# Performance work log

Hardware: AMD Instinct MI355X
Metric: run time of the kernel (lower is better)

The kernel has to match this reference:

```python
import jax, jax.numpy as jnp
import numpy as np

N, E, D, H = 100000, 1600000, 128, 128


def setup_inputs() -> dict:
    key = jax.random.key(0)
    ks = jax.random.split(key, 7)
    x = jax.random.normal(ks[0], (N, D), dtype=jnp.float32)
    edge_index = jax.random.randint(ks[1], (2, E), 0, N, dtype=jnp.int64)
    edge_weight = jax.random.uniform(ks[2], (E,), dtype=jnp.float32)
    s = 1.0 / np.sqrt(D)
    W0 = jax.random.normal(ks[3], (D, H), dtype=jnp.float32) * s
    b0 = jnp.zeros((H,), dtype=jnp.float32)
    W1 = jax.random.normal(ks[4], (H, H), dtype=jnp.float32) * (1.0 / np.sqrt(H))
    b1 = jnp.zeros((H,), dtype=jnp.float32)
    return {"x": x, "edge_weight": edge_weight, "W0": W0, "b0": b0,
            "W1": W1, "b1": b1, "edge_index": edge_index}


def reference(x, edge_weight, W0, b0, W1, b1, edge_index):
    src, dst = edge_index[0], edge_index[1]
    n = x.shape[0]
    # gcn_norm with self-loops (fill_value=1): deg includes the self-loop weight
    deg = jax.ops.segment_sum(edge_weight, dst, num_segments=n) + 1.0  # [N]
    dis = jnp.where(deg > 0, jax.lax.rsqrt(deg), 0.0)                  # deg^-1/2
    norm = dis[src] * edge_weight * dis[dst]                           # [E]
    self_coef = dis * dis                                              # self-loop norm = 1/deg

    def gcn_layer(h, W, b):
        hW = h @ W                                                     # [N,H]
        agg = jax.ops.segment_sum(norm[:, None] * hW[src], dst, num_segments=n)
        agg = agg + self_coef[:, None] * hW                            # self-loop term
        return jax.nn.relu(agg + b)

    h1 = gcn_layer(x, W0, b0)
    h2 = gcn_layer(h1, W1, b1)
    return jnp.concatenate([h1, h2], axis=1)  # [N, 2H]
```

## Files before the change

### kernel.cpp

```cpp
#include <hip/hip_runtime.h>
#include <hip/hip_fp16.h>


typedef unsigned int u32;
typedef _Float16 f16;
typedef f16 f16x8 __attribute__((ext_vector_type(8)));
typedef float f32x4 __attribute__((ext_vector_type(4)));

__global__ __launch_bounds__(256) void k_wfrag(const float* __restrict__ W0,
                                               const float* __restrict__ W1,
                                               __half* __restrict__ Wf) {
    int idx = blockIdx.x * 256 + threadIdx.x;
    const float* W = (idx < 2048) ? W0 : W1;
    int id = idx & 2047;
    int l = id & 63, nt = (id >> 6) & 7, ks = id >> 9;
    int nn = nt * 16 + (l & 15);
    int kb = ks * 32 + ((l >> 4) & 3) * 4;
    union { int4 v; __half h[8]; } pk;
#pragma unroll
    for (int j = 0; j < 8; ++j) {
        int k = kb + (j & 3) + 16 * (j >> 2);
        pk.h[j] = __float2half(W[k * 128 + nn]);
    }
    *(int4*)(Wf + (size_t)idx * 8) = pk.v;
}

__device__ __forceinline__ void gemm_body(const float* __restrict__ A, int lda,
                                          const __half* __restrict__ Wf,
                                          __half* __restrict__ C, int n,
                                          int bid, int t) {
    const int w2 = t >> 6, l = t & 63;
    const int node = bid * 64 + w2 * 16 + (l & 15);
    const int koff = ((l >> 4) & 3) * 4;
    const bool ok = node < n;
    const float* ap = A + (size_t)(ok ? node : 0) * lda;

    f16x8 af[4];
#pragma unroll
    for (int ks = 0; ks < 4; ++ks) {
        float4 a0 = make_float4(0.f, 0.f, 0.f, 0.f), a1 = a0;
        if (ok) {
            a0 = *(const float4*)(ap + ks * 32 + koff);
            a1 = *(const float4*)(ap + ks * 32 + koff + 16);
        }
        f16x8 h;
        h[0] = (f16)a0.x; h[1] = (f16)a0.y; h[2] = (f16)a0.z; h[3] = (f16)a0.w;
        h[4] = (f16)a1.x; h[5] = (f16)a1.y; h[6] = (f16)a1.z; h[7] = (f16)a1.w;
        af[ks] = h;
    }

    f32x4 acc[8];
#pragma unroll
    for (int i = 0; i < 8; ++i) acc[i] = (f32x4){0.f, 0.f, 0.f, 0.f};

#pragma unroll
    for (int ks = 0; ks < 4; ++ks) {
#pragma unroll
        for (int nt = 0; nt < 8; ++nt) {
            f16x8 wf = *(const f16x8*)(Wf + ((size_t)(ks * 8 + nt) * 64 + l) * 8);
            acc[nt] = __builtin_amdgcn_mfma_f32_16x16x32_f16(wf, af[ks], acc[nt], 0, 0, 0);
        }
    }

    if (ok) {
        const int c0 = ((l >> 4) & 3) * 4;
#pragma unroll
        for (int nt = 0; nt < 8; ++nt) {
            union { short4 s4; __half h[4]; } pk;
#pragma unroll
            for (int r2 = 0; r2 < 4; ++r2) pk.h[r2] = __float2half(acc[nt][r2]);
            *(short4*)(C + (size_t)node * 128 + nt * 16 + c0) = pk.s4;
        }
    }
}

__global__ __launch_bounds__(256) void k_p1gemm(const int* __restrict__ dst,
                                                u32* __restrict__ H,
                                                int e, int NB, int nch,
                                                const float* __restrict__ A, int lda,
                                                const __half* __restrict__ Wf,
                                                __half* __restrict__ C, int n) {
    const int bid = blockIdx.x, t = threadIdx.x;
    if (bid >= nch) {
        gemm_body(A, lda, Wf, C, n, bid - nch, t);
        return;
    }
    __shared__ u32 lcnt[512];
    lcnt[t] = 0; lcnt[t + 256] = 0;
    __syncthreads();
    int i0 = bid * 4096 + t;
#pragma unroll
    for (int u = 0; u < 16; ++u) {
        int i = i0 + u * 256;
        if (i < e) atomicAdd(&lcnt[(u32)dst[i] >> 9], 1u);
    }
    __syncthreads();
    for (int b = t; b < NB; b += 256) H[(size_t)b * nch + bid] = lcnt[b];
}

__global__ __launch_bounds__(256) void k_scan1(u32* data, u32* sums, int n) {
    __shared__ u32 tmp[256];
    int gid = blockIdx.x * 256 + threadIdx.x;
    u32 v = (gid < n) ? data[gid] : 0;
    tmp[threadIdx.x] = v;
    __syncthreads();
    for (int off = 1; off < 256; off <<= 1) {
        u32 t = (threadIdx.x >= off) ? tmp[threadIdx.x - off] : 0;
        __syncthreads();
        tmp[threadIdx.x] += t;
        __syncthreads();
    }
    if (gid < n) data[gid] = tmp[threadIdx.x] - v;
    if (threadIdx.x == 255) sums[blockIdx.x] = tmp[255];
}

__global__ __launch_bounds__(512) void k_scan2(u32* sums, int nb) {
    __shared__ u32 tmp[512];
    u32 v = (threadIdx.x < nb) ? sums[threadIdx.x] : 0;
    tmp[threadIdx.x] = v;
    __syncthreads();
    for (int off = 1; off < 512; off <<= 1) {
        u32 t = (threadIdx.x >= off) ? tmp[threadIdx.x - off] : 0;
        __syncthreads();
        tmp[threadIdx.x] += t;
        __syncthreads();
    }
    if (threadIdx.x < nb) sums[threadIdx.x] = tmp[threadIdx.x] - v;
}

__global__ __launch_bounds__(256) void k_scan3(u32* data, const u32* sums, int n) {
    int gid = blockIdx.x * 256 + threadIdx.x;
    if (gid < n) data[gid] += sums[blockIdx.x];
}

__global__ __launch_bounds__(256) void k_p2(const int* __restrict__ src,
                                            const int* __restrict__ dst,
                                            const float* __restrict__ w,
                                            const u32* __restrict__ H,
                                            int2* __restrict__ tmp,
                                            int e, int NB, int nch) {
    __shared__ u32 lcnt[512];
    __shared__ u32 lbase[512];
    const int t = threadIdx.x, bid = blockIdx.x;
    lcnt[t] = 0; lcnt[t + 256] = 0;
    __syncthreads();
    for (int b = t; b < NB; b += 256) lbase[b] = H[(size_t)b * nch + bid];
    __syncthreads();
    int i0 = bid * 4096 + t;
#pragma unroll
    for (int u = 0; u < 16; ++u) {
        int i = i0 + u * 256;
        if (i < e) {
            int d = dst[i];
            u32 b = (u32)d >> 9;
            u32 lr = atomicAdd(&lcnt[b], 1u);
            tmp[lbase[b] + lr] = make_int2(src[i] | ((d & 511) << 17),
                                           __float_as_int(w[i]));
        }
    }
}

__global__ __launch_bounds__(512) void k_p3a(const int2* __restrict__ tmp,
                                             const u32* __restrict__ H,
                                             int* __restrict__ rowstart,
                                             float* __restrict__ dis,
                                             int e, int n, int NB, int nch) {
    const int bid = blockIdx.x, t = threadIdx.x;
    __shared__ u32 cnt[512];
    __shared__ u32 degx[512];
    __shared__ u32 stmp[512];

    cnt[t] = 0; degx[t] = 0;
    __syncthreads();

    const int bs = (int)H[(size_t)bid * nch];
    const int be = (bid + 1 < NB) ? (int)H[(size_t)(bid + 1) * nch] : e;

    for (int j = bs + t; j < be; j += 512) {
        int2 r = tmp[j];
        u32 low = ((u32)r.x >> 17) & 511u;
        atomicAdd(&cnt[low], 1u);
        atomicAdd(&degx[low], (u32)(__int_as_float(r.y) * 1048576.0f + 0.5f));
    }
    __syncthreads();

    u32 v = cnt[t];
    stmp[t] = v;
    __syncthreads();
    for (int o = 1; o < 512; o <<= 1) {
        u32 x = (t >= o) ? stmp[t - o] : 0u;
        __syncthreads();
        stmp[t] += x;
        __syncthreads();
    }

    const int node = bid * 512 + t;
    if (node < n) {
        rowstart[node] = bs + (int)(stmp[t] - v);
        dis[node] = rsqrtf(1.0f + (float)degx[t] * (1.0f / 1048576.0f));
    }
}

__global__ __launch_bounds__(512) void k_p3b(const int2* __restrict__ tmp,
                                             const u32* __restrict__ H,
                                             const int* __restrict__ rowstart,
                                             const float* __restrict__ dis,
                                             int2* __restrict__ ep,
                                             int e, int n, int NB, int nch) {
    const int bid = blockIdx.x, t = threadIdx.x;
    __shared__ u32 cur[512];
    const int node = bid * 512 + t;
    cur[t] = (node < n) ? (u32)rowstart[node] : 0u;
    __syncthreads();

    const int bs = (int)H[(size_t)bid * nch];
    const int be = (bid + 1 < NB) ? (int)H[(size_t)(bid + 1) * nch] : e;

    for (int j = bs + t; j < be; j += 512) {
        int2 r = tmp[j];
        u32 low = ((u32)r.x >> 17) & 511u;
        int s = r.x & 0x1FFFF;
        float wd = __int_as_float(r.y) * dis[s];
        u32 p = atomicAdd(&cur[low], 1u);
        ep[p] = make_int2(s, __float_as_int(wd));
    }
}

__global__ __launch_bounds__(256) void k_gemm(const float* __restrict__ A, int lda,
                                              const __half* __restrict__ Wf,
                                              __half* __restrict__ C, int n) {
    gemm_body(A, lda, Wf, C, n, blockIdx.x, threadIdx.x);
}

__global__ __launch_bounds__(256) void k_agg(const __half* __restrict__ hW,
                                             const int2* __restrict__ ep,
                                             const int* __restrict__ rowstart,
                                             const float* __restrict__ dis,
                                             const float* __restrict__ bias,
                                             float* __restrict__ outcol,
                                             int n, int e) {
    int wid = blockIdx.x * 4 + (threadIdx.x >> 6);
    int lane = threadIdx.x & 63;
    if (wid >= n) return;

    int start = rowstart[wid];
    int end   = (wid == n - 1) ? e : rowstart[wid + 1];
    start = __builtin_amdgcn_readfirstlane(start);
    end   = __builtin_amdgcn_readfirstlane(end);

    const float dd = dis[wid];
    float2 h = __half22float2(*(const __half2*)(hW + (size_t)wid * 128 + lane * 2));
    float2 acc;
    acc.x = dd * h.x;
    acc.y = dd * h.y;

    int j = start;
    for (; j + 15 < end; j += 16) {
        int2 r[16];
        __half2 v[16];
#pragma unroll
        for (int u = 0; u < 16; ++u) r[u] = ep[j + u];
#pragma unroll
        for (int u = 0; u < 16; ++u)
            v[u] = *(const __half2*)(hW + (size_t)r[u].x * 128 + lane * 2);
#pragma unroll
        for (int u = 0; u < 16; ++u) {
            float nm = __int_as_float(r[u].y);
            float2 f = __half22float2(v[u]);
            acc.x += nm * f.x;
            acc.y += nm * f.y;
        }
    }
    for (; j + 7 < end; j += 8) {
        int2 r[8];
        __half2 v[8];
#pragma unroll
        for (int u = 0; u < 8; ++u) r[u] = ep[j + u];
#pragma unroll
        for (int u = 0; u < 8; ++u)
            v[u] = *(const __half2*)(hW + (size_t)r[u].x * 128 + lane * 2);
#pragma unroll
        for (int u = 0; u < 8; ++u) {
            float nm = __int_as_float(r[u].y);
            float2 f = __half22float2(v[u]);
            acc.x += nm * f.x;
            acc.y += nm * f.y;
        }
    }
    for (; j + 3 < end; j += 4) {
        int2 r[4];
        __half2 v[4];
#pragma unroll
        for (int u = 0; u < 4; ++u) r[u] = ep[j + u];
#pragma unroll
        for (int u = 0; u < 4; ++u)
            v[u] = *(const __half2*)(hW + (size_t)r[u].x * 128 + lane * 2);
#pragma unroll
        for (int u = 0; u < 4; ++u) {
            float nm = __int_as_float(r[u].y);
            float2 f = __half22float2(v[u]);
            acc.x += nm * f.x;
            acc.y += nm * f.y;
        }
    }
    for (; j < end; ++j) {
        int2 rec = ep[j];
        float nm = __int_as_float(rec.y);
        float2 v = __half22float2(*(const __half2*)(hW + (size_t)rec.x * 128 + lane * 2));
        acc.x += nm * v.x;
        acc.y += nm * v.y;
    }

    float2 b = *(const float2*)(bias + lane * 2);
    float2 o;
    o.x = fmaxf(dd * acc.x + b.x, 0.f);
    o.y = fmaxf(dd * acc.y + b.y, 0.f);
    *(float2*)(outcol + (size_t)wid * 256 + lane * 2) = o;
}

extern "C" void kernel_launch(void* const* d_in, const int* in_sizes, int n_in,
                              void* d_out, int out_size, void* d_ws, size_t ws_size,
                              hipStream_t stream) {
    const float* x  = (const float*)d_in[0];
    const float* ew = (const float*)d_in[1];
    const float* W0 = (const float*)d_in[2];
    const float* b0 = (const float*)d_in[3];
    const float* W1 = (const float*)d_in[4];
    const float* b1 = (const float*)d_in[5];
    const int*   ei = (const int*)d_in[6];

    const int N = in_sizes[0] / 128;
    const int E = in_sizes[1];
    const int* src = ei;
    const int* dst = ei + E;
    float* out = (float*)d_out;

    const int NB  = (N + 511) >> 9;
    const int nch = (E + 4095) >> 12;
    const int scanN = NB * nch;
    const int scanB = (scanN + 255) / 256;
    const int gT = (N + 63) / 64;
    const int gA = (N + 3) / 4;

    const size_t Hsz = (size_t)((scanN + 1) & ~1);
    const size_t Npad = (size_t)((N + 1) & ~1);
    u32*   H        = (u32*)d_ws;
    int*   rowstart = (int*)(H + Hsz);
    float* dis      = (float*)(rowstart + Npad);
    int2*  tmp      = (int2*)(dis + Npad);
    int2*  ep       = tmp + E;
    __half* hW      = (__half*)(ep + E);
    __half* Wf      = hW + (size_t)N * 128;
    u32*   sums     = (u32*)(Wf + 32768);

    k_wfrag<<<16, 256, 0, stream>>>(W0, W1, Wf);
    k_p1gemm<<<nch + gT, 256, 0, stream>>>(dst, H, E, NB, nch, x, 128, Wf, hW, N);
    k_scan1<<<scanB, 256, 0, stream>>>(H, sums, scanN);
    k_scan2<<<1, 512, 0, stream>>>(sums, scanB);
    k_scan3<<<scanB, 256, 0, stream>>>(H, sums, scanN);
    k_p2<<<nch, 256, 0, stream>>>(src, dst, ew, H, tmp, E, NB, nch);
    k_p3a<<<NB, 512, 0, stream>>>(tmp, H, rowstart, dis, E, N, NB, nch);
    k_p3b<<<NB, 512, 0, stream>>>(tmp, H, rowstart, dis, ep, E, N, NB, nch);

    k_agg<<<gA, 256, 0, stream>>>(hW, ep, rowstart, dis, b0, out, N, E);

    k_gemm<<<gT, 256, 0, stream>>>(out, 256, Wf + 16384, hW, N);
    k_agg<<<gA, 256, 0, stream>>>(hW, ep, rowstart, dis, b1, out + 128, N, E);
}
```

Measured before the change: 272.3 us.

## Fuse layer-1 aggregation with layer-2 GEMM and fold scan fixup into consumers

Layer-1 aggregation now runs in a kernel that keeps each block's 16 output rows in shared memory as fp16 and immediately multiplies them by W1 with MFMA. This removes the separate GEMM launch and its reread of the fp32 layer-1 output. The third scan pass is dropped, and consumers instead add the block sum S[idx>>8] when they read H. Layer-2 hW is written into the reused tmp buffer. The fused kernel runs the GEMM at small tiles of 16 rows, and its gather phase has less parallelism per block.

```diff
diff --git a/kernel.cpp b/kernel.cpp
--- a/kernel.cpp
+++ b/kernel.cpp
@@ -4,6 +4,7 @@
 
 typedef unsigned int u32;
 typedef _Float16 f16;
+typedef f16 f16x4 __attribute__((ext_vector_type(4)));
 typedef f16 f16x8 __attribute__((ext_vector_type(8)));
 typedef float f32x4 __attribute__((ext_vector_type(4)));
 
@@ -128,15 +129,11 @@
     if (threadIdx.x < nb) sums[threadIdx.x] = tmp[threadIdx.x] - v;
 }
 
-__global__ __launch_bounds__(256) void k_scan3(u32* data, const u32* sums, int n) {
-    int gid = blockIdx.x * 256 + threadIdx.x;
-    if (gid < n) data[gid] += sums[blockIdx.x];
-}
-
 __global__ __launch_bounds__(256) void k_p2(const int* __restrict__ src,
                                             const int* __restrict__ dst,
                                             const float* __restrict__ w,
                                             const u32* __restrict__ H,
+                                            const u32* __restrict__ S,
                                             int2* __restrict__ tmp,
                                             int e, int NB, int nch) {
     __shared__ u32 lcnt[512];
@@ -144,7 +141,10 @@
     const int t = threadIdx.x, bid = blockIdx.x;
     lcnt[t] = 0; lcnt[t + 256] = 0;
     __syncthreads();
-    for (int b = t; b < NB; b += 256) lbase[b] = H[(size_t)b * nch + bid];
+    for (int b = t; b < NB; b += 256) {
+        u32 idx = (u32)b * nch + bid;
+        lbase[b] = H[idx] + S[idx >> 8];
+    }
     __syncthreads();
     int i0 = bid * 4096 + t;
 #pragma unroll
@@ -162,6 +162,7 @@
 
 __global__ __launch_bounds__(512) void k_p3a(const int2* __restrict__ tmp,
                                              const u32* __restrict__ H,
+                                             const u32* __restrict__ S,
                                              int* __restrict__ rowstart,
                                              float* __restrict__ dis,
                                              int e, int n, int NB, int nch) {
@@ -173,8 +174,10 @@
     cnt[t] = 0; degx[t] = 0;
     __syncthreads();
 
-    const int bs = (int)H[(size_t)bid * nch];
-    const int be = (bid + 1 < NB) ? (int)H[(size_t)(bid + 1) * nch] : e;
+    u32 i0 = (u32)bid * nch;
+    const int bs = (int)(H[i0] + S[i0 >> 8]);
+    u32 i1 = (u32)(bid + 1) * nch;
+    const int be = (bid + 1 < NB) ? (int)(H[i1] + S[i1 >> 8]) : e;
 
     for (int j = bs + t; j < be; j += 512) {
         int2 r = tmp[j];
@@ -203,6 +206,7 @@
 
 __global__ __launch_bounds__(512) void k_p3b(const int2* __restrict__ tmp,
                                              const u32* __restrict__ H,
+                                             const u32* __restrict__ S,
                                              const int* __restrict__ rowstart,
                                              const float* __restrict__ dis,
                                              int2* __restrict__ ep,
@@ -213,8 +217,10 @@
     cur[t] = (node < n) ? (u32)rowstart[node] : 0u;
     __syncthreads();
 
-    const int bs = (int)H[(size_t)bid * nch];
-    const int be = (bid + 1 < NB) ? (int)H[(size_t)(bid + 1) * nch] : e;
+    u32 i0 = (u32)bid * nch;
+    const int bs = (int)(H[i0] + S[i0 >> 8]);
+    u32 i1 = (u32)(bid + 1) * nch;
+    const int be = (bid + 1 < NB) ? (int)(H[i1] + S[i1 >> 8]) : e;
 
     for (int j = bs + t; j < be; j += 512) {
         int2 r = tmp[j];
@@ -226,10 +232,145 @@
     }
 }
 
-__global__ __launch_bounds__(256) void k_gemm(const float* __restrict__ A, int lda,
-                                              const __half* __restrict__ Wf,
-                                              __half* __restrict__ C, int n) {
-    gemm_body(A, lda, Wf, C, n, blockIdx.x, threadIdx.x);
+__device__ __forceinline__ float2 agg_row(const __half* __restrict__ hW, int ldh,
+                                          const int2* __restrict__ ep,
+                                          int start, int end, int lane,
+                                          float2 acc) {
+    int j = start;
+    for (; j + 15 < end; j += 16) {
+        int2 r[16];
+        __half2 v[16];
+#pragma unroll
+        for (int u = 0; u < 16; ++u) r[u] = ep[j + u];
+#pragma unroll
+        for (int u = 0; u < 16; ++u)
+            v[u] = *(const __half2*)(hW + (size_t)r[u].x * ldh + lane * 2);
+#pragma unroll
+        for (int u = 0; u < 16; ++u) {
+            float nm = __int_as_float(r[u].y);
+            float2 f = __half22float2(v[u]);
+            acc.x += nm * f.x;
+            acc.y += nm * f.y;
+        }
+    }
+    for (; j + 7 < end; j += 8) {
+        int2 r[8];
+        __half2 v[8];
+#pragma unroll
+        for (int u = 0; u < 8; ++u) r[u] = ep[j + u];
+#pragma unroll
+        for (int u = 0; u < 8; ++u)
+            v[u] = *(const __half2*)(hW + (size_t)r[u].x * ldh + lane * 2);
+#pragma unroll
+        for (int u = 0; u < 8; ++u) {
+            float nm = __int_as_float(r[u].y);
+            float2 f = __half22float2(v[u]);
+            acc.x += nm * f.x;
+            acc.y += nm * f.y;
+        }
+    }
+    for (; j + 3 < end; j += 4) {
+        int2 r[4];
+        __half2 v[4];
+#pragma unroll
+        for (int u = 0; u < 4; ++u) r[u] = ep[j + u];
+#pragma unroll
+        for (int u = 0; u < 4; ++u)
+            v[u] = *(const __half2*)(hW + (size_t)r[u].x * ldh + lane * 2);
+#pragma unroll
+        for (int u = 0; u < 4; ++u) {
+            float nm = __int_as_float(r[u].y);
+            float2 f = __half22float2(v[u]);
+            acc.x += nm * f.x;
+            acc.y += nm * f.y;
+        }
+    }
+    for (; j < end; ++j) {
+        int2 rec = ep[j];
+        float nm = __int_as_float(rec.y);
+        float2 v = __half22float2(*(const __half2*)(hW + (size_t)rec.x * ldh + lane * 2));
+        acc.x += nm * v.x;
+        acc.y += nm * v.y;
+    }
+    return acc;
+}
+
+__global__ __launch_bounds__(256) void k_aggemm(const __half* __restrict__ hW1,
+                                                const int2* __restrict__ ep,
+                                                const int* __restrict__ rowstart,
+                                                const float* __restrict__ dis,
+                                                const float* __restrict__ bias,
+                                                float* __restrict__ outcol,
+                                                const __half* __restrict__ Wf2,
+                                                __half* __restrict__ hW2,
+                                                int n, int e) {
+    __shared__ f16 As[16][132];
+    const int t = threadIdx.x;
+    const int w2 = t >> 6, lane = t & 63;
+
+    float2 b = *(const float2*)(bias + lane * 2);
+
+#pragma unroll
+    for (int i = 0; i < 4; ++i) {
+        const int lr = w2 * 4 + i;
+        const int wid = blockIdx.x * 16 + lr;
+        if (wid < n) {
+            int start = rowstart[wid];
+            int end   = (wid == n - 1) ? e : rowstart[wid + 1];
+            start = __builtin_amdgcn_readfirstlane(start);
+            end   = __builtin_amdgcn_readfirstlane(end);
+
+            const float dd = dis[wid];
+            float2 h = __half22float2(*(const __half2*)(hW1 + (size_t)wid * 128 + lane * 2));
+            float2 acc;
+            acc.x = dd * h.x;
+            acc.y = dd * h.y;
+            acc = agg_row(hW1, 128, ep, start, end, lane, acc);
+
+            float ox = fmaxf(dd * acc.x + b.x, 0.f);
+            float oy = fmaxf(dd * acc.y + b.y, 0.f);
+            *(float2*)(outcol + (size_t)wid * 256 + lane * 2) = make_float2(ox, oy);
+            As[lr][2 * lane]     = (f16)ox;
+            As[lr][2 * lane + 1] = (f16)oy;
+        } else {
+            As[lr][2 * lane]     = (f16)0.f;
+            As[lr][2 * lane + 1] = (f16)0.f;
+        }
+    }
+    __syncthreads();
+
+    const int koff = ((lane >> 4) & 3) * 4;
+    f32x4 acc2[2];
+    acc2[0] = (f32x4){0.f, 0.f, 0.f, 0.f};
+    acc2[1] = (f32x4){0.f, 0.f, 0.f, 0.f};
+
+#pragma unroll
+    for (int ks = 0; ks < 4; ++ks) {
+        f16x4 lo = *(const f16x4*)&As[lane & 15][ks * 32 + koff];
+        f16x4 hi = *(const f16x4*)&As[lane & 15][ks * 32 + koff + 16];
+        f16x8 af;
+        af[0] = lo[0]; af[1] = lo[1]; af[2] = lo[2]; af[3] = lo[3];
+        af[4] = hi[0]; af[5] = hi[1]; af[6] = hi[2]; af[7] = hi[3];
+#pragma unroll
+        for (int q = 0; q < 2; ++q) {
+            const int nt = w2 * 2 + q;
+            f16x8 wf = *(const f16x8*)(Wf2 + ((size_t)(ks * 8 + nt) * 64 + lane) * 8);
+            acc2[q] = __builtin_amdgcn_mfma_f32_16x16x32_f16(wf, af, acc2[q], 0, 0, 0);
+        }
+    }
+
+    const int node = blockIdx.x * 16 + (lane & 15);
+    if (node < n) {
+        const int c0 = ((lane >> 4) & 3) * 4;
+#pragma unroll
+        for (int q = 0; q < 2; ++q) {
+            const int nt = w2 * 2 + q;
+            union { short4 s4; __half h[4]; } pk;
+#pragma unroll
+            for (int r2 = 0; r2 < 4; ++r2) pk.h[r2] = __float2half(acc2[q][r2]);
+            *(short4*)(hW2 + (size_t)node * 128 + nt * 16 + c0) = pk.s4;
+        }
+    }
 }
 
 __global__ __launch_bounds__(256) void k_agg(const __half* __restrict__ hW,
@@ -253,63 +394,7 @@
     float2 acc;
     acc.x = dd * h.x;
     acc.y = dd * h.y;
-
-    int j = start;
-    for (; j + 15 < end; j += 16) {
-        int2 r[16];
-        __half2 v[16];
-#pragma unroll
-        for (int u = 0; u < 16; ++u) r[u] = ep[j + u];
-#pragma unroll
-        for (int u = 0; u < 16; ++u)
-            v[u] = *(const __half2*)(hW + (size_t)r[u].x * 128 + lane * 2);
-#pragma unroll
-        for (int u = 0; u < 16; ++u) {
-            float nm = __int_as_float(r[u].y);
-            float2 f = __half22float2(v[u]);
-            acc.x += nm * f.x;
-            acc.y += nm * f.y;
-        }
-    }
-    for (; j + 7 < end; j += 8) {
-        int2 r[8];
-        __half2 v[8];
-#pragma unroll
-        for (int u = 0; u < 8; ++u) r[u] = ep[j + u];
-#pragma unroll
-        for (int u = 0; u < 8; ++u)
-            v[u] = *(const __half2*)(hW + (size_t)r[u].x * 128 + lane * 2);
-#pragma unroll
-        for (int u = 0; u < 8; ++u) {
-            float nm = __int_as_float(r[u].y);
-            float2 f = __half22float2(v[u]);
-            acc.x += nm * f.x;
-            acc.y += nm * f.y;
-        }
-    }
-    for (; j + 3 < end; j += 4) {
-        int2 r[4];
-        __half2 v[4];
-#pragma unroll
-        for (int u = 0; u < 4; ++u) r[u] = ep[j + u];
-#pragma unroll
-        for (int u = 0; u < 4; ++u)
-            v[u] = *(const __half2*)(hW + (size_t)r[u].x * 128 + lane * 2);
-#pragma unroll
-        for (int u = 0; u < 4; ++u) {
-            float nm = __int_as_float(r[u].y);
-            float2 f = __half22float2(v[u]);
-            acc.x += nm * f.x;
-            acc.y += nm * f.y;
-        }
-    }
-    for (; j < end; ++j) {
-        int2 rec = ep[j];
-        float nm = __int_as_float(rec.y);
-        float2 v = __half22float2(*(const __half2*)(hW + (size_t)rec.x * 128 + lane * 2));
-        acc.x += nm * v.x;
-        acc.y += nm * v.y;
-    }
+    acc = agg_row(hW, 128, ep, start, end, lane, acc);
 
     float2 b = *(const float2*)(bias + lane * 2);
     float2 o;
@@ -340,30 +425,31 @@
     const int scanN = NB * nch;
     const int scanB = (scanN + 255) / 256;
     const int gT = (N + 63) / 64;
+    const int gF = (N + 15) / 16;
     const int gA = (N + 3) / 4;
 
-    const size_t Hsz = (size_t)((scanN + 1) & ~1);
+    const size_t Hsz  = (size_t)((scanN + 1) & ~1);
     const size_t Npad = (size_t)((N + 1) & ~1);
     u32*   H        = (u32*)d_ws;
-    int*   rowstart = (int*)(H + Hsz);
+    u32*   sums     = H + Hsz;
+    int*   rowstart = (int*)(sums + 512);
     float* dis      = (float*)(rowstart + Npad);
-    int2*  tmp      = (int2*)(dis + Npad);
-    int2*  ep       = tmp + E;
-    __half* hW      = (__half*)(ep + E);
-    __half* Wf      = hW + (size_t)N * 128;
-    u32*   sums     = (u32*)(Wf + 32768);
+    int2*  ep       = (int2*)(dis + Npad);
+    __half* hW1     = (__half*)(ep + E);
+    __half* Wf      = hW1 + (size_t)N * 128;
+    int2*  tmp      = (int2*)(Wf + 32768);
+    __half* hW2     = (__half*)tmp;
 
     k_wfrag<<<16, 256, 0, stream>>>(W0, W1, Wf);
-    k_p1gemm<<<nch + gT, 256, 0, stream>>>(dst, H, E, NB, nch, x, 128, Wf, hW, N);
+    k_p1gemm<<<nch + gT, 256, 0, stream>>>(dst, H, E, NB, nch, x, 128, Wf, hW1, N);
     k_scan1<<<scanB, 256, 0, stream>>>(H, sums, scanN);
     k_scan2<<<1, 512, 0, stream>>>(sums, scanB);
-    k_scan3<<<scanB, 256, 0, stream>>>(H, sums, scanN);
-    k_p2<<<nch, 256, 0, stream>>>(src, dst, ew, H, tmp, E, NB, nch);
-    k_p3a<<<NB, 512, 0, stream>>>(tmp, H, rowstart, dis, E, N, NB, nch);
-    k_p3b<<<NB, 512, 0, stream>>>(tmp, H, rowstart, dis, ep, E, N, NB, nch);
-
-    k_agg<<<gA, 256, 0, stream>>>(hW, ep, rowstart, dis, b0, out, N, E);
-
-    k_gemm<<<gT, 256, 0, stream>>>(out, 256, Wf + 16384, hW, N);
-    k_agg<<<gA, 256, 0, stream>>>(hW, ep, rowstart, dis, b1, out + 128, N, E);
-}
+    k_p2<<<nch, 256, 0, stream>>>(src, dst, ew, H, sums, tmp, E, NB, nch);
+    k_p3a<<<NB, 512, 0, stream>>>(tmp, H, sums, rowstart, dis, E, N, NB, nch);
+    k_p3b<<<NB, 512, 0, stream>>>(tmp, H, sums, rowstart, dis, ep, E, N, NB, nch);
+
+    k_aggemm<<<gF, 256, 0, stream>>>(hW1, ep, rowstart, dis, b0, out,
+                                     Wf + 16384, hW2, N, E);
+
+    k_agg<<<gA, 256, 0, stream>>>(hW2, ep, rowstart, dis, b1, out + 128, N, E);
+}
```

After: 260.0 us, median of 2. 4.5% less time.
